# Performance work log

Hardware: AMD Instinct MI355X
Metric: run time of the kernel (lower is better)

The kernel has to match this reference:

```python
import jax, jax.numpy as jnp
import numpy as np

B, N, M, D = 8, 4096, 256, 1024
H, HD, ROT = 16, 64, 32  # heads, head_dim, rotary dim (partial_rotary_factor=0.5)
GRID_H = GRID_W = 64     # sqrt(N)
BASE = 10000


def rope_tables_2d(h, w, rot_dim, base=BASE, dtype=jnp.float32):
    # 2D rope: half the rotary channels encode height, half encode width.
    n_freq = rot_dim // 4
    inv = 1.0 / (base ** (jnp.arange(n_freq, dtype=jnp.float32) / n_freq))
    fh = jnp.arange(h, dtype=jnp.float32)[:, None] * inv          # [h, nf]
    fw = jnp.arange(w, dtype=jnp.float32)[:, None] * inv          # [w, nf]
    fh_g = jnp.broadcast_to(fh[:, None, :], (h, w, n_freq))
    fw_g = jnp.broadcast_to(fw[None, :, :], (h, w, n_freq))
    freqs = jnp.concatenate([fh_g, fw_g], -1).reshape(h * w, rot_dim // 2)
    emb = jnp.concatenate([freqs, freqs], -1)                     # [h*w, rot_dim]
    return jnp.cos(emb).astype(dtype), jnp.sin(emb).astype(dtype)


def rotate_half(x):
    x1, x2 = jnp.split(x, 2, axis=-1)
    return jnp.concatenate([-x2, x1], axis=-1)


def layernorm(x, w, b, eps=1e-5):
    mu = x.mean(-1, keepdims=True)
    var = ((x - mu) ** 2).mean(-1, keepdims=True)
    return (x - mu) * jax.lax.rsqrt(var + eps) * w + b


def setup_inputs() -> dict:
    key = jax.random.key(0)
    ks = jax.random.split(key, 5)
    inner = H * HD
    return {
        "x": jax.random.normal(ks[0], (B, N, D), jnp.float32),
        "latents": jax.random.normal(ks[1], (B, M, D), jnp.float32),
        "ln_x_w": jnp.ones((D,), jnp.float32),
        "ln_x_b": jnp.zeros((D,), jnp.float32),
        "ln_l_w": jnp.ones((D,), jnp.float32),
        "ln_l_b": jnp.zeros((D,), jnp.float32),
        "Wq": jax.random.normal(ks[2], (D, inner), jnp.float32) * (D ** -0.5),
        "Wkv": jax.random.normal(ks[3], (D, 2 * inner), jnp.float32) * (D ** -0.5),
        "Wo": jax.random.normal(ks[4], (inner, D), jnp.float32) * (inner ** -0.5),
    }


def reference(x, latents, ln_x_w, ln_x_b, ln_l_w, ln_l_b, Wq, Wkv, Wo):
    scale = HD ** -0.5
    xn = layernorm(x, ln_x_w, ln_x_b)
    ln = layernorm(latents, ln_l_w, ln_l_b)

    q = ln @ Wq                                   # [B, M, H*HD]
    kv_x = xn @ Wkv                               # [B, N, 2*H*HD]
    kv_l = ln @ Wkv                               # [B, M, 2*H*HD]
    k_x, v_x = jnp.split(kv_x, 2, axis=-1)
    k_l, v_l = jnp.split(kv_l, 2, axis=-1)

    def to_bhnd(t, L):
        return t.reshape(t.shape[0], L, H, HD).transpose(0, 2, 1, 3)

    q = to_bhnd(q, M)                             # [B, H, M, HD]
    k_x = to_bhnd(k_x, N)                         # [B, H, N, HD]
    v_x = to_bhnd(v_x, N)
    k_l = to_bhnd(k_l, M)
    v_l = to_bhnd(v_l, M)

    # partial 2D RoPE on input keys only (first ROT channels)
    cos, sin = rope_tables_2d(GRID_H, GRID_W, ROT)  # [N, ROT]
    k_rope, k_pass = k_x[..., :ROT], k_x[..., ROT:]
    k_rope = k_rope * cos + rotate_half(k_rope) * sin
    k_x = jnp.concatenate([k_rope, k_pass], axis=-1)

    k = jnp.concatenate([k_x, k_l], axis=2)       # [B, H, N+M, HD]
    v = jnp.concatenate([v_x, v_l], axis=2)

    sim = jnp.einsum('bhid,bhjd->bhij', q * scale, k)   # [B, H, M, N+M]
    attn = jax.nn.softmax(sim, axis=-1)
    out = jnp.einsum('bhij,bhjd->bhid', attn, v)        # [B, H, M, HD]
    out = out.transpose(0, 2, 1, 3).reshape(out.shape[0], M, H * HD)
    return out @ Wo                                      # [B, M, D]
```

## Files before the change

kernel.cpp:

```cpp
#include <hip/hip_runtime.h>
#include <hip/hip_bf16.h>

#define Bb 8
#define Nn 4096
#define Mm 256
#define Dd 1024
#define Hh 16
#define HDd 64
#define Ss 4352
#define INNERd 1024
#define SPLIT 8

typedef __attribute__((ext_vector_type(4))) float f32x4;
typedef __attribute__((ext_vector_type(8))) short short8;
typedef __attribute__((ext_vector_type(4))) int int4v;

__device__ __forceinline__ float bf2f(short u) {
  union { unsigned int i; float f; } c;
  c.i = ((unsigned int)(unsigned short)u) << 16;
  return c.f;
}
__device__ __forceinline__ short f2bf(float f) {
  union { float f; unsigned int i; } c; c.f = f;
  unsigned int x = c.i;
  x += 0x7fff + ((x >> 16) & 1);
  return (short)(x >> 16);
}
__device__ __forceinline__ void gload16(const short* g, short* l) {
  __builtin_amdgcn_global_load_lds(
      (const __attribute__((address_space(1))) void*)g,
      (__attribute__((address_space(3))) void*)l, 16, 0, 0);
}

__global__ void ln_bf16_kernel(const float* __restrict__ src,
                               const float* __restrict__ w,
                               const float* __restrict__ bvec,
                               short* __restrict__ dst) {
  int row = blockIdx.x;
  const float4* x4 = (const float4*)(src + (size_t)row * Dd);
  int t = threadIdx.x;
  float4 v = x4[t];
  float s  = v.x + v.y + v.z + v.w;
  float ss = v.x*v.x + v.y*v.y + v.z*v.z + v.w*v.w;
#pragma unroll
  for (int o = 1; o < 64; o <<= 1) {
    s  += __shfl_xor(s,  o, 64);
    ss += __shfl_xor(ss, o, 64);
  }
  __shared__ float red[8];
  int wv = t >> 6;
  if ((t & 63) == 0) { red[wv] = s; red[4 + wv] = ss; }
  __syncthreads();
  float tot  = red[0] + red[1] + red[2] + red[3];
  float tot2 = red[4] + red[5] + red[6] + red[7];
  float mean = tot * (1.0f / Dd);
  float var  = tot2 * (1.0f / Dd) - mean * mean;
  float inv  = rsqrtf(var + 1e-5f);
  float4 wv4 = ((const float4*)w)[t];
  float4 bv4 = ((const float4*)bvec)[t];
  short4 o4;
  o4.x = f2bf((v.x - mean) * inv * wv4.x + bv4.x);
  o4.y = f2bf((v.y - mean) * inv * wv4.y + bv4.y);
  o4.z = f2bf((v.z - mean) * inv * wv4.z + bv4.z);
  o4.w = f2bf((v.w - mean) * inv * wv4.w + bv4.w);
  *(short4*)(dst + (size_t)row * Dd + t * 4) = o4;
}

__global__ void wconv_kernel(const float* __restrict__ src, short* __restrict__ dst,
                             int K, int Ncol) {
  __shared__ float tile[32][33];
  int bx = blockIdx.x, by = blockIdx.y;
  int tx = threadIdx.x, ty = threadIdx.y;
#pragma unroll
  for (int i = 0; i < 32; i += 8)
    tile[ty + i][tx] = src[(size_t)(by * 32 + ty + i) * Ncol + bx * 32 + tx];
  __syncthreads();
#pragma unroll
  for (int i = 0; i < 32; i += 8)
    dst[(size_t)(bx * 32 + ty + i) * K + by * 32 + tx] = f2bf(tile[tx][ty + i]);
}

template<int MODE>
__global__ __launch_bounds__(256, 4) void gemm_bt_kernel(
    const short* __restrict__ A, const short* __restrict__ Bt,
    void* __restrict__ C0, short* __restrict__ kdst, short* __restrict__ vdst,
    int ncp) {
  __shared__ __align__(16) short Asm[128 * 64];
  __shared__ __align__(16) short Bsm[128 * 64];
  __shared__ float ctab[(MODE == 2) ? 1024 : 1];
  int t = threadIdx.x;
  int wave = t >> 6, lane = t & 63;
  int wm = (wave >> 1) * 64, wn = (wave & 1) * 64;
  int lr = lane & 15, lg = lane >> 4;
  int nwg = gridDim.x;
  int cpx = nwg >> 3;
  int swz = (blockIdx.x & 7) * cpx + (blockIdx.x >> 3);
  int colp = swz % ncp, rowp = swz / ncp;
  int brow = rowp * 128, bcol = colp * 128;
  if (MODE == 2) {
#pragma unroll
    for (int i = t; i < 512; i += 256) {
      int pos = i >> 3, f = i & 7;
      float ang = (float)pos * exp2f(-1.6609640474436813f * (float)f);
      ctab[i] = cosf(ang);
      ctab[512 + i] = sinf(ang);
    }
  }
  f32x4 acc[4][4] = {};
  for (int kt = 0; kt < 1024; kt += 64) {
    __syncthreads();
#pragma unroll
    for (int u = 0; u < 4; u++) {
      int cid = t + u * 256;
      int r = cid >> 3, c = cid & 7;
      int cl = c ^ (r & 7);
      gload16(A + (size_t)(brow + r) * 1024 + kt + cl * 8, Asm + cid * 8);
      gload16(Bt + (size_t)(bcol + r) * 1024 + kt + cl * 8, Bsm + cid * 8);
    }
    __syncthreads();
#pragma unroll
    for (int ks = 0; ks < 2; ks++) {
      short8 a[4], b[4];
#pragma unroll
      for (int i = 0; i < 4; i++) {
        int ra = wm + i * 16 + lr;
        a[i] = *(const short8*)(Asm + ra * 64 + (((ks * 4 + lg) ^ (ra & 7)) * 8));
        int rb = wn + i * 16 + lr;
        b[i] = *(const short8*)(Bsm + rb * 64 + (((ks * 4 + lg) ^ (rb & 7)) * 8));
      }
#pragma unroll
      for (int mi = 0; mi < 4; mi++)
#pragma unroll
        for (int ni = 0; ni < 4; ni++)
          acc[mi][ni] = __builtin_amdgcn_mfma_f32_16x16x32_bf16(a[mi], b[ni], acc[mi][ni], 0, 0, 0);
    }
  }
  int cbase = bcol + wn;
  bool kreg = (cbase & 2047) < 1024;
#pragma unroll
  for (int mi = 0; mi < 4; mi++)
#pragma unroll
    for (int rr = 0; rr < 4; rr++) {
      int row = brow + wm + mi * 16 + lg * 4 + rr;
      float v[4];
#pragma unroll
      for (int ni = 0; ni < 4; ni++) v[ni] = acc[mi][ni][rr];
      if (MODE == 0) {
        float* C = (float*)C0;
#pragma unroll
        for (int ni = 0; ni < 4; ni++)
          C[(size_t)row * 1024 + cbase + ni * 16 + lr] = v[ni];
      } else if (MODE == 2) {
        int bb = row >> 12, n = row & 4095;
        if (kreg) {
          int pos = (lr & 8) ? (n & 63) : (n >> 6);
          float cs = ctab[pos * 8 + (lr & 7)];
          float sn = ctab[512 + pos * 8 + (lr & 7)];
          float v0 = v[0], v1 = v[1];
          v[0] = v0 * cs - v1 * sn;
          v[1] = v1 * cs + v0 * sn;
        }
        short* dstp = kreg ? kdst : vdst;
        int h = (cbase & 1023) >> 6;
        size_t rb = (((size_t)(bb * Hh + h)) * Ss + n) * HDd;
#pragma unroll
        for (int ni = 0; ni < 4; ni++)
          dstp[rb + ni * 16 + lr] = f2bf(v[ni]);
      } else {
        int bb = row >> 8, m = row & 255;
        if (cbase < 1024) {
          int h = cbase >> 6;
          size_t rb = (((size_t)(bb * Hh + h)) * Mm + m) * HDd;
#pragma unroll
          for (int ni = 0; ni < 4; ni++)
            ((short*)C0)[rb + ni * 16 + lr] = f2bf(v[ni] * 0.125f);
        } else if (cbase < 2048) {
          int h = (cbase - 1024) >> 6;
          size_t rb = (((size_t)(bb * Hh + h)) * Ss + (Nn + m)) * HDd;
#pragma unroll
          for (int ni = 0; ni < 4; ni++)
            kdst[rb + ni * 16 + lr] = f2bf(v[ni]);
        } else {
          int h = (cbase - 2048) >> 6;
          size_t rb = (((size_t)(bb * Hh + h)) * Ss + (Nn + m)) * HDd;
#pragma unroll
          for (int ni = 0; ni < 4; ni++)
            vdst[rb + ni * 16 + lr] = f2bf(v[ni]);
        }
      }
    }
}

__global__ __launch_bounds__(512) void attn_kernel(const short* __restrict__ qb,
                            const short* __restrict__ kb,
                            const short* __restrict__ vb,
                            float* __restrict__ pO,
                            float* __restrict__ pS) {
  __shared__ __align__(16) short Ksm[64 * 64];
  __shared__ __align__(16) short Vsm[64 * 64];
  int blk = blockIdx.x;
  int sp = blk & (SPLIT - 1), bh = blk >> 3;
  int t = threadIdx.x, wave = t >> 6, lane = t & 63;
  int lr = lane & 15, lg = lane >> 4;
  int q0 = wave * 32;
  const short* qptr = qb + (size_t)bh * Mm * HDd;
  short8 qf[2][2];
#pragma unroll
  for (int qi = 0; qi < 2; qi++)
#pragma unroll
    for (int ks = 0; ks < 2; ks++)
      qf[qi][ks] = *(const short8*)(qptr + (size_t)(q0 + qi * 16 + lr) * HDd + ks * 32 + lg * 8);
  f32x4 accOT[4][2] = {};
  float psq[2] = {0.0f, 0.0f};
  const short* kbase = kb + (size_t)bh * Ss * HDd;
  const short* vbase = vb + (size_t)bh * Ss * HDd;
  int tile0 = (sp * 68) >> 3, tile1 = ((sp + 1) * 68) >> 3;
  for (int tt = tile0; tt < tile1; tt++) {
    int kt = tt * 64;
    __syncthreads();
    {
      int r = t >> 3, c = t & 7;
      int cl = c ^ (r & 7);
      gload16(kbase + (size_t)(kt + r) * HDd + cl * 8, Ksm + t * 8);
      short8 vv = *(const short8*)(vbase + (size_t)(kt + r) * HDd + c * 8);
      int sc = ((r >> 5) << 2) | ((r >> 2) & 3);
      int sw = (((r >> 4) & 1) << 2) | (r & 3);
#pragma unroll
      for (int e = 0; e < 8; e++) {
        int d = c * 8 + e;
        Vsm[d * 64 + ((sc ^ (d & 7)) * 8) + sw] = vv[e];
      }
    }
    __syncthreads();
    f32x4 accST[4][2] = {};
#pragma unroll
    for (int ks = 0; ks < 2; ks++) {
      short8 ka[4];
#pragma unroll
      for (int ji = 0; ji < 4; ji++) {
        int j = ji * 16 + lr;
        int cd = ks * 4 + lg;
        ka[ji] = *(const short8*)(Ksm + j * 64 + ((cd ^ (j & 7)) * 8));
      }
#pragma unroll
      for (int ji = 0; ji < 4; ji++)
#pragma unroll
        for (int qi = 0; qi < 2; qi++)
          accST[ji][qi] = __builtin_amdgcn_mfma_f32_16x16x32_bf16(ka[ji], qf[qi][ks], accST[ji][qi], 0, 0, 0);
    }
    short8 pb[2][2];
#pragma unroll
    for (int qi = 0; qi < 2; qi++) {
#pragma unroll
      for (int ji = 0; ji < 4; ji++)
#pragma unroll
        for (int r = 0; r < 4; r++) {
          float pv = __expf(accST[ji][qi][r]);
          accST[ji][qi][r] = pv;
          psq[qi] += pv;
        }
#pragma unroll
      for (int s = 0; s < 2; s++)
#pragma unroll
        for (int r = 0; r < 4; r++) {
          pb[s][qi][r]     = f2bf(accST[2 * s][qi][r]);
          pb[s][qi][4 + r] = f2bf(accST[2 * s + 1][qi][r]);
        }
    }
#pragma unroll
    for (int s = 0; s < 2; s++) {
      short8 va[4];
#pragma unroll
      for (int di = 0; di < 4; di++) {
        int d = di * 16 + lr;
        int ck = s * 4 + lg;
        va[di] = *(const short8*)(Vsm + d * 64 + ((ck ^ (d & 7)) * 8));
      }
#pragma unroll
      for (int di = 0; di < 4; di++)
#pragma unroll
        for (int qi = 0; qi < 2; qi++)
          accOT[di][qi] = __builtin_amdgcn_mfma_f32_16x16x32_bf16(va[di], pb[s][qi], accOT[di][qi], 0, 0, 0);
    }
  }
#pragma unroll
  for (int qi = 0; qi < 2; qi++) {
    psq[qi] += __shfl_xor(psq[qi], 16, 64);
    psq[qi] += __shfl_xor(psq[qi], 32, 64);
  }
  size_t base = (size_t)blk * 256;
  if (lane < 16) {
#pragma unroll
    for (int qi = 0; qi < 2; qi++)
      pS[base + q0 + qi * 16 + lr] = psq[qi];
  }
  float* poB = pO + base * 64;
#pragma unroll
  for (int di = 0; di < 4; di++)
#pragma unroll
    for (int qi = 0; qi < 2; qi++)
#pragma unroll
      for (int r = 0; r < 4; r++)
        poB[(size_t)(di * 16 + lg * 4 + r) * 256 + q0 + qi * 16 + lr] = accOT[di][qi][r];
}

__global__ void attn_combine(const float* __restrict__ pO, const float* __restrict__ pS,
                             short* __restrict__ ob) {
  int blk = blockIdx.x;
  int bh = blk >> 1, dh = (blk & 1) << 5;
  int q = threadIdx.x;
  float den = 0.0f;
  float acc[32] = {};
#pragma unroll
  for (int s = 0; s < SPLIT; s++) {
    size_t b2 = (size_t)(bh * SPLIT + s);
    den += pS[b2 * 256 + q];
    const float* po = pO + b2 * 16384 + (size_t)dh * 256;
#pragma unroll
    for (int d = 0; d < 32; d++) acc[d] += po[d * 256 + q];
  }
  float rden = 1.0f / den;
  int b = bh >> 4, h = bh & 15;
  short* dst = ob + ((size_t)(b * Mm + q)) * INNERd + h * HDd + dh;
#pragma unroll
  for (int c = 0; c < 4; c++) {
    short8 o8;
#pragma unroll
    for (int e = 0; e < 8; e++) o8[e] = f2bf(acc[c * 8 + e] * rden);
    *(short8*)(dst + c * 8) = o8;
  }
}

extern "C" void kernel_launch(void* const* d_in, const int* in_sizes, int n_in,
                              void* d_out, int out_size, void* d_ws, size_t ws_size,
                              hipStream_t stream) {
  const float* x    = (const float*)d_in[0];
  const float* lat  = (const float*)d_in[1];
  const float* lnxw = (const float*)d_in[2];
  const float* lnxb = (const float*)d_in[3];
  const float* lnlw = (const float*)d_in[4];
  const float* lnlb = (const float*)d_in[5];
  const float* Wq   = (const float*)d_in[6];
  const float* Wkv  = (const float*)d_in[7];
  const float* Wo   = (const float*)d_in[8];
  char* w = (char*)d_ws;
  const size_t MB = 1048576;
  short* Wqkvt = (short*)(w + 0 * MB);
  short* Wot   = (short*)(w + 6 * MB);
  short* xn    = (short*)(w + 8 * MB);
  short* lnr   = (short*)(w + 72 * MB);
  short* qbuf  = (short*)(w + 76 * MB);
  short* kbuf  = (short*)(w + 80 * MB);
  short* vbuf  = (short*)(w + 148 * MB);
  short* aout  = (short*)(w + 216 * MB);
  float* pO    = (float*)(w + 8 * MB);
  float* pS    = (float*)(w + 72 * MB);

  ln_bf16_kernel<<<dim3(Bb * Nn), dim3(256), 0, stream>>>(x, lnxw, lnxb, xn);
  ln_bf16_kernel<<<dim3(Bb * Mm), dim3(256), 0, stream>>>(lat, lnlw, lnlb, lnr);
  wconv_kernel<<<dim3(32, 32), dim3(32, 8), 0, stream>>>(Wq, Wqkvt, 1024, 1024);
  wconv_kernel<<<dim3(64, 32), dim3(32, 8), 0, stream>>>(Wkv, Wqkvt + (size_t)1024 * 1024, 1024, 2048);
  wconv_kernel<<<dim3(32, 32), dim3(32, 8), 0, stream>>>(Wo, Wot, 1024, 1024);
  gemm_bt_kernel<2><<<dim3(4096), dim3(256), 0, stream>>>(
      xn, Wqkvt + (size_t)1024 * 1024, nullptr, kbuf, vbuf, 16);
  gemm_bt_kernel<4><<<dim3(384), dim3(256), 0, stream>>>(
      lnr, Wqkvt, (void*)qbuf, kbuf, vbuf, 24);
  attn_kernel<<<dim3(Bb * Hh * SPLIT), dim3(512), 0, stream>>>(qbuf, kbuf, vbuf, pO, pS);
  attn_combine<<<dim3(256), dim3(256), 0, stream>>>(pO, pS, aout);
  gemm_bt_kernel<0><<<dim3(128), dim3(256), 0, stream>>>(
      aout, Wot, d_out, nullptr, nullptr, 8);
}
```

Before: 314.0 us.

## Merge prep and projection launches, fold log2e into Q, store attention partials as bf16

Measured after the change: 304.5 us, median of 2. -3.0%, faster.

```diff
diff --git a/kernel.cpp b/kernel.cpp
--- a/kernel.cpp
+++ b/kernel.cpp
@@ -32,62 +32,186 @@
       (__attribute__((address_space(3))) void*)l, 16, 0, 0);
 }
 
-__global__ void ln_bf16_kernel(const float* __restrict__ src,
-                               const float* __restrict__ w,
-                               const float* __restrict__ bvec,
-                               short* __restrict__ dst) {
-  int row = blockIdx.x;
-  const float4* x4 = (const float4*)(src + (size_t)row * Dd);
-  int t = threadIdx.x;
-  float4 v = x4[t];
-  float s  = v.x + v.y + v.z + v.w;
-  float ss = v.x*v.x + v.y*v.y + v.z*v.z + v.w*v.w;
-#pragma unroll
-  for (int o = 1; o < 64; o <<= 1) {
-    s  += __shfl_xor(s,  o, 64);
-    ss += __shfl_xor(ss, o, 64);
-  }
-  __shared__ float red[8];
-  int wv = t >> 6;
-  if ((t & 63) == 0) { red[wv] = s; red[4 + wv] = ss; }
-  __syncthreads();
-  float tot  = red[0] + red[1] + red[2] + red[3];
-  float tot2 = red[4] + red[5] + red[6] + red[7];
-  float mean = tot * (1.0f / Dd);
-  float var  = tot2 * (1.0f / Dd) - mean * mean;
-  float inv  = rsqrtf(var + 1e-5f);
-  float4 wv4 = ((const float4*)w)[t];
-  float4 bv4 = ((const float4*)bvec)[t];
-  short4 o4;
-  o4.x = f2bf((v.x - mean) * inv * wv4.x + bv4.x);
-  o4.y = f2bf((v.y - mean) * inv * wv4.y + bv4.y);
-  o4.z = f2bf((v.z - mean) * inv * wv4.z + bv4.z);
-  o4.w = f2bf((v.w - mean) * inv * wv4.w + bv4.w);
-  *(short4*)(dst + (size_t)row * Dd + t * 4) = o4;
-}
-
-__global__ void wconv_kernel(const float* __restrict__ src, short* __restrict__ dst,
-                             int K, int Ncol) {
-  __shared__ float tile[32][33];
-  int bx = blockIdx.x, by = blockIdx.y;
-  int tx = threadIdx.x, ty = threadIdx.y;
-#pragma unroll
-  for (int i = 0; i < 32; i += 8)
-    tile[ty + i][tx] = src[(size_t)(by * 32 + ty + i) * Ncol + bx * 32 + tx];
-  __syncthreads();
-#pragma unroll
-  for (int i = 0; i < 32; i += 8)
-    dst[(size_t)(bx * 32 + ty + i) * K + by * 32 + tx] = f2bf(tile[tx][ty + i]);
-}
-
-template<int MODE>
-__global__ __launch_bounds__(256, 4) void gemm_bt_kernel(
-    const short* __restrict__ A, const short* __restrict__ Bt,
-    void* __restrict__ C0, short* __restrict__ kdst, short* __restrict__ vdst,
-    int ncp) {
+__global__ __launch_bounds__(256) void prep_kernel(
+    const float* __restrict__ x, const float* __restrict__ lat,
+    const float* __restrict__ lnxw, const float* __restrict__ lnxb,
+    const float* __restrict__ lnlw, const float* __restrict__ lnlb,
+    const float* __restrict__ Wq, const float* __restrict__ Wkv,
+    const float* __restrict__ Wo,
+    short* __restrict__ xn, short* __restrict__ lnr,
+    short* __restrict__ Wqkvt, short* __restrict__ Wot) {
+  __shared__ float shbuf[32 * 33];
+  int b = blockIdx.x, t = threadIdx.x;
+  if (b < 34816) {
+    const float *src, *w, *bv; short* dst; int row;
+    if (b < 32768) { src = x;   w = lnxw; bv = lnxb; dst = xn;  row = b; }
+    else           { src = lat; w = lnlw; bv = lnlb; dst = lnr; row = b - 32768; }
+    const float4* x4 = (const float4*)(src + (size_t)row * Dd);
+    float4 v = x4[t];
+    float s  = v.x + v.y + v.z + v.w;
+    float ss = v.x*v.x + v.y*v.y + v.z*v.z + v.w*v.w;
+#pragma unroll
+    for (int o = 1; o < 64; o <<= 1) {
+      s  += __shfl_xor(s,  o, 64);
+      ss += __shfl_xor(ss, o, 64);
+    }
+    int wv = t >> 6;
+    if ((t & 63) == 0) { shbuf[wv] = s; shbuf[4 + wv] = ss; }
+    __syncthreads();
+    float tot  = shbuf[0] + shbuf[1] + shbuf[2] + shbuf[3];
+    float tot2 = shbuf[4] + shbuf[5] + shbuf[6] + shbuf[7];
+    float mean = tot * (1.0f / Dd);
+    float var  = tot2 * (1.0f / Dd) - mean * mean;
+    float inv  = rsqrtf(var + 1e-5f);
+    float4 wv4 = ((const float4*)w)[t];
+    float4 bv4 = ((const float4*)bv)[t];
+    short4 o4;
+    o4.x = f2bf((v.x - mean) * inv * wv4.x + bv4.x);
+    o4.y = f2bf((v.y - mean) * inv * wv4.y + bv4.y);
+    o4.z = f2bf((v.z - mean) * inv * wv4.z + bv4.z);
+    o4.w = f2bf((v.w - mean) * inv * wv4.w + bv4.w);
+    *(short4*)(dst + (size_t)row * Dd + t * 4) = o4;
+  } else {
+    int tb = b - 34816;
+    const float* src; short* dst; int Ncol, bx, by;
+    if (tb < 1024)      { src = Wq;  dst = Wqkvt; Ncol = 1024; bx = tb & 31; by = tb >> 5; }
+    else if (tb < 3072) { int u = tb - 1024; src = Wkv; dst = Wqkvt + (size_t)1024 * 1024; Ncol = 2048; bx = u & 63; by = u >> 6; }
+    else                { int u = tb - 3072; src = Wo;  dst = Wot; Ncol = 1024; bx = u & 31; by = u >> 5; }
+    int tx = t & 31, ty = t >> 5;
+#pragma unroll
+    for (int i = 0; i < 32; i += 8)
+      shbuf[(ty + i) * 33 + tx] = src[(size_t)(by * 32 + ty + i) * Ncol + bx * 32 + tx];
+    __syncthreads();
+#pragma unroll
+    for (int i = 0; i < 32; i += 8)
+      dst[(size_t)(bx * 32 + ty + i) * 1024 + by * 32 + tx] = f2bf(shbuf[tx * 33 + ty + i]);
+  }
+}
+
+__global__ __launch_bounds__(256, 4) void gemm_fused_kernel(
+    const short* __restrict__ xn, const short* __restrict__ lnr,
+    const short* __restrict__ Wkvt, const short* __restrict__ Wqkvt,
+    short* __restrict__ qdst, short* __restrict__ kdst, short* __restrict__ vdst) {
   __shared__ __align__(16) short Asm[128 * 64];
   __shared__ __align__(16) short Bsm[128 * 64];
-  __shared__ float ctab[(MODE == 2) ? 1024 : 1];
+  __shared__ float ctab[1024];
+  int t = threadIdx.x;
+  int wave = t >> 6, lane = t & 63;
+  int wm = (wave >> 1) * 64, wn = (wave & 1) * 64;
+  int lr = lane & 15, lg = lane >> 4;
+  bool big = (int)blockIdx.x < 4096;
+  const short* A  = big ? xn  : lnr;
+  const short* Bt = big ? Wkvt : Wqkvt;
+  int bid = big ? blockIdx.x : blockIdx.x - 4096;
+  int nwg = big ? 4096 : 384;
+  int ncp = big ? 16 : 24;
+  int cpx = nwg >> 3;
+  int swz = (bid & 7) * cpx + (bid >> 3);
+  int colp = swz % ncp, rowp = swz / ncp;
+  int brow = rowp * 128, bcol = colp * 128;
+  if (big) {
+#pragma unroll
+    for (int i = t; i < 512; i += 256) {
+      int pos = i >> 3, f = i & 7;
+      float ang = (float)pos * exp2f(-1.6609640474436813f * (float)f);
+      ctab[i] = cosf(ang);
+      ctab[512 + i] = sinf(ang);
+    }
+  }
+  f32x4 acc[4][4] = {};
+  for (int kt = 0; kt < 1024; kt += 64) {
+    __syncthreads();
+#pragma unroll
+    for (int u = 0; u < 4; u++) {
+      int cid = t + u * 256;
+      int r = cid >> 3, c = cid & 7;
+      int cl = c ^ (r & 7);
+      gload16(A + (size_t)(brow + r) * 1024 + kt + cl * 8, Asm + cid * 8);
+      gload16(Bt + (size_t)(bcol + r) * 1024 + kt + cl * 8, Bsm + cid * 8);
+    }
+    __syncthreads();
+#pragma unroll
+    for (int ks = 0; ks < 2; ks++) {
+      short8 a[4], b[4];
+#pragma unroll
+      for (int i = 0; i < 4; i++) {
+        int ra = wm + i * 16 + lr;
+        a[i] = *(const short8*)(Asm + ra * 64 + (((ks * 4 + lg) ^ (ra & 7)) * 8));
+        int rb = wn + i * 16 + lr;
+        b[i] = *(const short8*)(Bsm + rb * 64 + (((ks * 4 + lg) ^ (rb & 7)) * 8));
+      }
+#pragma unroll
+      for (int mi = 0; mi < 4; mi++)
+#pragma unroll
+        for (int ni = 0; ni < 4; ni++)
+          acc[mi][ni] = __builtin_amdgcn_mfma_f32_16x16x32_bf16(a[mi], b[ni], acc[mi][ni], 0, 0, 0);
+    }
+  }
+  int cbase = bcol + wn;
+  if (big) {
+    bool kreg = cbase < 1024;
+    short* dstp = kreg ? kdst : vdst;
+    int h = (cbase & 1023) >> 6;
+#pragma unroll
+    for (int mi = 0; mi < 4; mi++)
+#pragma unroll
+      for (int rr = 0; rr < 4; rr++) {
+        int row = brow + wm + mi * 16 + lg * 4 + rr;
+        int bb = row >> 12, n = row & 4095;
+        float v[4];
+#pragma unroll
+        for (int ni = 0; ni < 4; ni++) v[ni] = acc[mi][ni][rr];
+        if (kreg) {
+          int pos = (lr & 8) ? (n & 63) : (n >> 6);
+          float cs = ctab[pos * 8 + (lr & 7)];
+          float sn = ctab[512 + pos * 8 + (lr & 7)];
+          float v0 = v[0], v1 = v[1];
+          v[0] = v0 * cs - v1 * sn;
+          v[1] = v1 * cs + v0 * sn;
+        }
+        size_t rb = (((size_t)(bb * Hh + h)) * Ss + n) * HDd;
+#pragma unroll
+        for (int ni = 0; ni < 4; ni++)
+          dstp[rb + ni * 16 + lr] = f2bf(v[ni]);
+      }
+  } else {
+#pragma unroll
+    for (int mi = 0; mi < 4; mi++)
+#pragma unroll
+      for (int rr = 0; rr < 4; rr++) {
+        int row = brow + wm + mi * 16 + lg * 4 + rr;
+        int bb = row >> 8, m = row & 255;
+        float v[4];
+#pragma unroll
+        for (int ni = 0; ni < 4; ni++) v[ni] = acc[mi][ni][rr];
+        if (cbase < 1024) {
+          int h = cbase >> 6;
+          size_t rb = (((size_t)(bb * Hh + h)) * Mm + m) * HDd;
+#pragma unroll
+          for (int ni = 0; ni < 4; ni++)
+            qdst[rb + ni * 16 + lr] = f2bf(v[ni] * 0.18033688f);
+        } else if (cbase < 2048) {
+          int h = (cbase - 1024) >> 6;
+          size_t rb = (((size_t)(bb * Hh + h)) * Ss + (Nn + m)) * HDd;
+#pragma unroll
+          for (int ni = 0; ni < 4; ni++)
+            kdst[rb + ni * 16 + lr] = f2bf(v[ni]);
+        } else {
+          int h = (cbase - 2048) >> 6;
+          size_t rb = (((size_t)(bb * Hh + h)) * Ss + (Nn + m)) * HDd;
+#pragma unroll
+          for (int ni = 0; ni < 4; ni++)
+            vdst[rb + ni * 16 + lr] = f2bf(v[ni]);
+        }
+      }
+  }
+}
+
+__global__ __launch_bounds__(256, 4) void gemm_out_kernel(
+    const short* __restrict__ A, const short* __restrict__ Bt,
+    float* __restrict__ C, int ncp) {
+  __shared__ __align__(16) short Asm[128 * 64];
+  __shared__ __align__(16) short Bsm[128 * 64];
   int t = threadIdx.x;
   int wave = t >> 6, lane = t & 63;
   int wm = (wave >> 1) * 64, wn = (wave & 1) * 64;
@@ -97,15 +221,6 @@
   int swz = (blockIdx.x & 7) * cpx + (blockIdx.x >> 3);
   int colp = swz % ncp, rowp = swz / ncp;
   int brow = rowp * 128, bcol = colp * 128;
-  if (MODE == 2) {
-#pragma unroll
-    for (int i = t; i < 512; i += 256) {
-      int pos = i >> 3, f = i & 7;
-      float ang = (float)pos * exp2f(-1.6609640474436813f * (float)f);
-      ctab[i] = cosf(ang);
-      ctab[512 + i] = sinf(ang);
-    }
-  }
   f32x4 acc[4][4] = {};
   for (int kt = 0; kt < 1024; kt += 64) {
     __syncthreads();
@@ -135,66 +250,22 @@
           acc[mi][ni] = __builtin_amdgcn_mfma_f32_16x16x32_bf16(a[mi], b[ni], acc[mi][ni], 0, 0, 0);
     }
   }
-  int cbase = bcol + wn;
-  bool kreg = (cbase & 2047) < 1024;
 #pragma unroll
   for (int mi = 0; mi < 4; mi++)
 #pragma unroll
-    for (int rr = 0; rr < 4; rr++) {
-      int row = brow + wm + mi * 16 + lg * 4 + rr;
-      float v[4];
-#pragma unroll
-      for (int ni = 0; ni < 4; ni++) v[ni] = acc[mi][ni][rr];
-      if (MODE == 0) {
-        float* C = (float*)C0;
-#pragma unroll
-        for (int ni = 0; ni < 4; ni++)
-          C[(size_t)row * 1024 + cbase + ni * 16 + lr] = v[ni];
-      } else if (MODE == 2) {
-        int bb = row >> 12, n = row & 4095;
-        if (kreg) {
-          int pos = (lr & 8) ? (n & 63) : (n >> 6);
-          float cs = ctab[pos * 8 + (lr & 7)];
-          float sn = ctab[512 + pos * 8 + (lr & 7)];
-          float v0 = v[0], v1 = v[1];
-          v[0] = v0 * cs - v1 * sn;
-          v[1] = v1 * cs + v0 * sn;
-        }
-        short* dstp = kreg ? kdst : vdst;
-        int h = (cbase & 1023) >> 6;
-        size_t rb = (((size_t)(bb * Hh + h)) * Ss + n) * HDd;
-#pragma unroll
-        for (int ni = 0; ni < 4; ni++)
-          dstp[rb + ni * 16 + lr] = f2bf(v[ni]);
-      } else {
-        int bb = row >> 8, m = row & 255;
-        if (cbase < 1024) {
-          int h = cbase >> 6;
-          size_t rb = (((size_t)(bb * Hh + h)) * Mm + m) * HDd;
-#pragma unroll
-          for (int ni = 0; ni < 4; ni++)
-            ((short*)C0)[rb + ni * 16 + lr] = f2bf(v[ni] * 0.125f);
-        } else if (cbase < 2048) {
-          int h = (cbase - 1024) >> 6;
-          size_t rb = (((size_t)(bb * Hh + h)) * Ss + (Nn + m)) * HDd;
-#pragma unroll
-          for (int ni = 0; ni < 4; ni++)
-            kdst[rb + ni * 16 + lr] = f2bf(v[ni]);
-        } else {
-          int h = (cbase - 2048) >> 6;
-          size_t rb = (((size_t)(bb * Hh + h)) * Ss + (Nn + m)) * HDd;
-#pragma unroll
-          for (int ni = 0; ni < 4; ni++)
-            vdst[rb + ni * 16 + lr] = f2bf(v[ni]);
-        }
-      }
-    }
+    for (int ni = 0; ni < 4; ni++)
+#pragma unroll
+      for (int r = 0; r < 4; r++) {
+        int row = brow + wm + mi * 16 + lg * 4 + r;
+        int col = bcol + wn + ni * 16 + lr;
+        C[(size_t)row * 1024 + col] = acc[mi][ni][r];
+      }
 }
 
 __global__ __launch_bounds__(512) void attn_kernel(const short* __restrict__ qb,
                             const short* __restrict__ kb,
                             const short* __restrict__ vb,
-                            float* __restrict__ pO,
+                            short* __restrict__ pO,
                             float* __restrict__ pS) {
   __shared__ __align__(16) short Ksm[64 * 64];
   __shared__ __align__(16) short Vsm[64 * 64];
@@ -255,7 +326,7 @@
       for (int ji = 0; ji < 4; ji++)
 #pragma unroll
         for (int r = 0; r < 4; r++) {
-          float pv = __expf(accST[ji][qi][r]);
+          float pv = exp2f(accST[ji][qi][r]);
           accST[ji][qi][r] = pv;
           psq[qi] += pv;
         }
@@ -294,17 +365,17 @@
     for (int qi = 0; qi < 2; qi++)
       pS[base + q0 + qi * 16 + lr] = psq[qi];
   }
-  float* poB = pO + base * 64;
+  short* poB = pO + base * 64;
 #pragma unroll
   for (int di = 0; di < 4; di++)
 #pragma unroll
     for (int qi = 0; qi < 2; qi++)
 #pragma unroll
       for (int r = 0; r < 4; r++)
-        poB[(size_t)(di * 16 + lg * 4 + r) * 256 + q0 + qi * 16 + lr] = accOT[di][qi][r];
-}
-
-__global__ void attn_combine(const float* __restrict__ pO, const float* __restrict__ pS,
+        poB[(size_t)(di * 16 + lg * 4 + r) * 256 + q0 + qi * 16 + lr] = f2bf(accOT[di][qi][r]);
+}
+
+__global__ void attn_combine(const short* __restrict__ pO, const float* __restrict__ pS,
                              short* __restrict__ ob) {
   int blk = blockIdx.x;
   int bh = blk >> 1, dh = (blk & 1) << 5;
@@ -315,9 +386,9 @@
   for (int s = 0; s < SPLIT; s++) {
     size_t b2 = (size_t)(bh * SPLIT + s);
     den += pS[b2 * 256 + q];
-    const float* po = pO + b2 * 16384 + (size_t)dh * 256;
-#pragma unroll
-    for (int d = 0; d < 32; d++) acc[d] += po[d * 256 + q];
+    const short* po = pO + b2 * 16384 + (size_t)dh * 256;
+#pragma unroll
+    for (int d = 0; d < 32; d++) acc[d] += bf2f(po[d * 256 + q]);
   }
   float rden = 1.0f / den;
   int b = bh >> 4, h = bh & 15;
@@ -353,20 +424,14 @@
   short* kbuf  = (short*)(w + 80 * MB);
   short* vbuf  = (short*)(w + 148 * MB);
   short* aout  = (short*)(w + 216 * MB);
-  float* pO    = (float*)(w + 8 * MB);
+  short* pO    = (short*)(w + 8 * MB);
   float* pS    = (float*)(w + 72 * MB);
 
-  ln_bf16_kernel<<<dim3(Bb * Nn), dim3(256), 0, stream>>>(x, lnxw, lnxb, xn);
-  ln_bf16_kernel<<<dim3(Bb * Mm), dim3(256), 0, stream>>>(lat, lnlw, lnlb, lnr);
-  wconv_kernel<<<dim3(32, 32), dim3(32, 8), 0, stream>>>(Wq, Wqkvt, 1024, 1024);
-  wconv_kernel<<<dim3(64, 32), dim3(32, 8), 0, stream>>>(Wkv, Wqkvt + (size_t)1024 * 1024, 1024, 2048);
-  wconv_kernel<<<dim3(32, 32), dim3(32, 8), 0, stream>>>(Wo, Wot, 1024, 1024);
-  gemm_bt_kernel<2><<<dim3(4096), dim3(256), 0, stream>>>(
-      xn, Wqkvt + (size_t)1024 * 1024, nullptr, kbuf, vbuf, 16);
-  gemm_bt_kernel<4><<<dim3(384), dim3(256), 0, stream>>>(
-      lnr, Wqkvt, (void*)qbuf, kbuf, vbuf, 24);
+  prep_kernel<<<dim3(38912), dim3(256), 0, stream>>>(
+      x, lat, lnxw, lnxb, lnlw, lnlb, Wq, Wkv, Wo, xn, lnr, Wqkvt, Wot);
+  gemm_fused_kernel<<<dim3(4480), dim3(256), 0, stream>>>(
+      xn, lnr, Wqkvt + (size_t)1024 * 1024, Wqkvt, qbuf, kbuf, vbuf);
   attn_kernel<<<dim3(Bb * Hh * SPLIT), dim3(512), 0, stream>>>(qbuf, kbuf, vbuf, pO, pS);
   attn_combine<<<dim3(256), dim3(256), 0, stream>>>(pO, pS, aout);
-  gemm_bt_kernel<0><<<dim3(128), dim3(256), 0, stream>>>(
-      aout, Wot, d_out, nullptr, nullptr, 8);
-}
+  gemm_out_kernel<<<dim3(128), dim3(256), 0, stream>>>(aout, Wot, (float*)d_out, 8);
+}
```
